# Kernel tuning notes

Hardware: AMD Instinct MI355X
Metric: run time of the kernel (lower is better)

## Reference

```python
import jax, jax.numpy as jnp
import numpy as np

N = 8388608

def setup_inputs() -> dict:
    key = jax.random.key(0)
    k1, k2 = jax.random.split(key)
    preds = jax.random.normal(k1, (N, 5), dtype=jnp.float32)
    target = jax.random.normal(k2, (N, 3), dtype=jnp.float32)
    return {"preds": preds, "target": target}

def reference(preds, target):
    # main MSE over the first 3 quantile columns: [N, 3]
    main_mse = (preds[:, :3] - target[:, :3]) ** 2

    p2 = preds[:, 2]
    p3 = preds[:, 3]
    t2 = target[:, 2]

    # lower-range loss, vectorized form of the per-row if/elif/else: [N]
    lower = jnp.where(
        p3 > p2,
        jnp.float32(1000.0),
        jnp.where(p3 > t2 * 0.95, jnp.float32(0.0), (p3 - t2 * 0.95) ** 2),
    )

    # NOTE: the original code assigns upper_range_loss = torch.Tensor(lowe_range_loss),
    # i.e. the upper range loss is (buggily) a copy of the lower range loss.
    # We replicate that behavior faithfully.
    upper = lower

    # concatenate all loss elements (3N + N + N) and reduce with mean
    loss = jnp.concatenate([main_mse.ravel(), lower, upper])
    return jnp.mean(loss)
```

## Files before the change

### kernel.cpp

```cpp
#include <hip/hip_runtime.h>


#define NROWS 8388608
#define RPT 4
#define THREADS 256
#define GRID (NROWS / (RPT * THREADS))

typedef float v4f __attribute__((ext_vector_type(4)));

__global__ void __launch_bounds__(256) qloss_partial(
    const float* __restrict__ preds,
    const float* __restrict__ target,
    double* __restrict__ ws)
{
    const int t = threadIdx.x;
    const size_t g = (size_t)blockIdx.x * THREADS + t;

    const v4f* gp = (const v4f*)preds  + 5 * g;
    const v4f* gt = (const v4f*)target + 3 * g;

    v4f P[5], T[3];
    #pragma unroll
    for (int k = 0; k < 5; ++k) P[k] = gp[k];
    #pragma unroll
    for (int k = 0; k < 3; ++k) T[k] = gt[k];

    float sum = 0.0f;
    #pragma unroll
    for (int r = 0; r < RPT; ++r) {
        const float p0 = P[(5*r+0) >> 2][(5*r+0) & 3];
        const float p1 = P[(5*r+1) >> 2][(5*r+1) & 3];
        const float p2 = P[(5*r+2) >> 2][(5*r+2) & 3];
        const float p3 = P[(5*r+3) >> 2][(5*r+3) & 3];
        const float t0 = T[(3*r+0) >> 2][(3*r+0) & 3];
        const float t1 = T[(3*r+1) >> 2][(3*r+1) & 3];
        const float t2 = T[(3*r+2) >> 2][(3*r+2) & 3];

        const float a0 = p0 - t0;
        const float a1 = p1 - t1;
        const float a2 = p2 - t2;
        const float m  = a0*a0 + a1*a1 + a2*a2;

        const float q = t2 * 0.95f;
        const float d = p3 - q;
        const float lower = (p3 > p2) ? 1000.0f : ((p3 > q) ? 0.0f : d * d);

        sum += m + 2.0f * lower;
    }
    double acc = (double)sum;

    #pragma unroll
    for (int off = 32; off > 0; off >>= 1)
        acc += __shfl_down(acc, off, 64);

    __shared__ double red[4];
    const int lane = t & 63;
    const int wave = t >> 6;
    if (lane == 0) red[wave] = acc;
    __syncthreads();

    if (t == 0)
        ws[blockIdx.x] = red[0] + red[1] + red[2] + red[3];
}

__global__ void __launch_bounds__(256) qloss_final(
    const double* __restrict__ ws, float* __restrict__ out)
{
    const int t = threadIdx.x;
    double acc = 0.0;
    #pragma unroll
    for (int i = 0; i < GRID / 256; ++i)
        acc += ws[t + i * 256];

    #pragma unroll
    for (int off = 32; off > 0; off >>= 1)
        acc += __shfl_down(acc, off, 64);

    __shared__ double red[4];
    const int lane = t & 63;
    const int wave = t >> 6;
    if (lane == 0) red[wave] = acc;
    __syncthreads();

    if (t == 0)
        *out = (float)((red[0] + red[1] + red[2] + red[3]) / (5.0 * (double)NROWS));
}

extern "C" void kernel_launch(void* const* d_in, const int* in_sizes, int n_in,
                              void* d_out, int out_size, void* d_ws, size_t ws_size,
                              hipStream_t stream)
{
    const float* preds  = (const float*)d_in[0];
    const float* target = (const float*)d_in[1];
    float* out  = (float*)d_out;
    double* ws  = (double*)d_ws;

    qloss_partial<<<GRID, THREADS, 0, stream>>>(preds, target, ws);
    qloss_final<<<1, 256, 0, stream>>>(ws, out);
}
```

Baseline: 293.6 us.

## Use grid-stride loop with double-buffered register prefetch of row groups

Reduces the grid from 8192 to 2048 blocks, so each thread processes four 4-row groups in a grid-stride loop. The next group's loads are issued into a second register buffer before the current group is computed. The aim is more memory-level parallelism per thread and lower block launch and per-block reduction overhead. The cost is higher register use, which may lower occupancy; fewer blocks also means fewer waves to hide latency.

```diff
diff --git a/kernel.cpp b/kernel.cpp
--- a/kernel.cpp
+++ b/kernel.cpp
@@ -1,33 +1,32 @@
 #include <hip/hip_runtime.h>
 
 
-#define NROWS 8388608
-#define RPT 4
+#define NROWS   8388608
 #define THREADS 256
-#define GRID (NROWS / (RPT * THREADS))
+#define GRID    2048
+#define NGROUPS (NROWS / 4)
+#define GSTRIDE ((size_t)GRID * THREADS)
+#define GPT     4
 
 typedef float v4f __attribute__((ext_vector_type(4)));
 
-__global__ void __launch_bounds__(256) qloss_partial(
-    const float* __restrict__ preds,
-    const float* __restrict__ target,
-    double* __restrict__ ws)
+__device__ __forceinline__ void load_batch(const v4f* __restrict__ gp,
+                                           const v4f* __restrict__ gt,
+                                           size_t g, v4f P[5], v4f T[3])
 {
-    const int t = threadIdx.x;
-    const size_t g = (size_t)blockIdx.x * THREADS + t;
+    const v4f* p = gp + 5 * g;
+    const v4f* t = gt + 3 * g;
+    #pragma unroll
+    for (int k = 0; k < 5; ++k) P[k] = p[k];
+    #pragma unroll
+    for (int k = 0; k < 3; ++k) T[k] = t[k];
+}
 
-    const v4f* gp = (const v4f*)preds  + 5 * g;
-    const v4f* gt = (const v4f*)target + 3 * g;
-
-    v4f P[5], T[3];
-    #pragma unroll
-    for (int k = 0; k < 5; ++k) P[k] = gp[k];
-    #pragma unroll
-    for (int k = 0; k < 3; ++k) T[k] = gt[k];
-
+__device__ __forceinline__ float compute_batch(const v4f P[5], const v4f T[3])
+{
     float sum = 0.0f;
     #pragma unroll
-    for (int r = 0; r < RPT; ++r) {
+    for (int r = 0; r < 4; ++r) {
         const float p0 = P[(5*r+0) >> 2][(5*r+0) & 3];
         const float p1 = P[(5*r+1) >> 2][(5*r+1) & 3];
         const float p2 = P[(5*r+2) >> 2][(5*r+2) & 3];
@@ -47,7 +46,32 @@
 
         sum += m + 2.0f * lower;
     }
-    double acc = (double)sum;
+    return sum;
+}
+
+__global__ void __launch_bounds__(256) qloss_partial(
+    const float* __restrict__ preds,
+    const float* __restrict__ target,
+    double* __restrict__ ws)
+{
+    const int t = threadIdx.x;
+    const size_t g0 = (size_t)blockIdx.x * THREADS + t;
+
+    const v4f* gp = (const v4f*)preds;
+    const v4f* gt = (const v4f*)target;
+
+    v4f P[2][5], T[2][3];
+    load_batch(gp, gt, g0, P[0], T[0]);
+
+    double acc = 0.0;
+    #pragma unroll
+    for (int i = 0; i < GPT; ++i) {
+        const int cur = i & 1;
+        const int nxt = cur ^ 1;
+        if (i + 1 < GPT)
+            load_batch(gp, gt, g0 + (size_t)(i + 1) * GSTRIDE, P[nxt], T[nxt]);
+        acc += (double)compute_batch(P[cur], T[cur]);
+    }
 
     #pragma unroll
     for (int off = 32; off > 0; off >>= 1)
```

Result: no change. 297.7 us (+1.4%).
